# Kernel tuning notes

Measured on AMD Instinct MI355X. Metric: run time of the kernel, lower is better.

## Reference

```python
import jax, jax.numpy as jnp
import numpy as np

N = 100000   # nodes
E = 3200000  # edges (avg degree 32)
F = 128      # num_features
H = 256      # hidden_dim
D = 256      # embedding_dim
O = 2        # output_dim
BN_EPS = 1e-5


def _mk_layer(keys, fin, fmid, fout):
    kW1, kW2 = keys
    W1 = jax.random.normal(kW1, (fin, fmid), jnp.float32) / np.sqrt(fin)
    b1 = jnp.zeros((fmid,), jnp.float32)
    g = jnp.ones((fmid,), jnp.float32)
    be = jnp.zeros((fmid,), jnp.float32)
    mu = jnp.zeros((fmid,), jnp.float32)
    var = jnp.ones((fmid,), jnp.float32)
    W2 = jax.random.normal(kW2, (fmid, fout), jnp.float32) / np.sqrt(fmid)
    b2 = jnp.zeros((fout,), jnp.float32)
    return W1, b1, g, be, mu, var, W2, b2


def setup_inputs() -> dict:
    key = jax.random.key(0)
    ks = jax.random.split(key, 10)
    inp = {}
    inp["x"] = jax.random.normal(ks[0], (N, F), jnp.float32)
    inp["edge_index"] = jax.random.randint(ks[1], (2, E), 0, N, jnp.int32)
    names = ["W1", "b1", "g", "be", "mu", "var", "W2", "b2"]
    for pref, (fin, fmid, fout), kk in [
        ("l1", (F, H, H), (ks[2], ks[3])),
        ("l2", (H, H, H), (ks[4], ks[5])),
        ("l3", (H, H, D), (ks[6], ks[7])),
    ]:
        vals = _mk_layer(kk, fin, fmid, fout)
        for n, v in zip(names, vals):
            inp[f"{pref}_{n}"] = v
    inp["out_W"] = jax.random.normal(ks[8], (D, O), jnp.float32) / np.sqrt(D)
    inp["out_b"] = jnp.zeros((O,), jnp.float32)
    return inp


def gin_layer(h, src, dst, W1, b1, g, be, mu, var, W2, b2, final_relu):
    # GINConv (eps=0): z_i = x_i + sum_{j->i} x_j, then MLP(Linear-BN-ReLU-Linear[-ReLU])
    agg = jax.ops.segment_sum(h[src], dst, num_segments=N)
    z = h + agg
    z = z @ W1 + b1
    z = (z - mu) * jax.lax.rsqrt(var + BN_EPS) * g + be  # BatchNorm1d (inference)
    z = jax.nn.relu(z)
    z = z @ W2 + b2
    if final_relu:
        z = jax.nn.relu(z)
    return z


def reference(x, edge_index,
              l1_W1, l1_b1, l1_g, l1_be, l1_mu, l1_var, l1_W2, l1_b2,
              l2_W1, l2_b1, l2_g, l2_be, l2_mu, l2_var, l2_W2, l2_b2,
              l3_W1, l3_b1, l3_g, l3_be, l3_mu, l3_var, l3_W2, l3_b2,
              out_W, out_b):
    src, dst = edge_index[0], edge_index[1]
    h = gin_layer(x, src, dst, l1_W1, l1_b1, l1_g, l1_be, l1_mu, l1_var, l1_W2, l1_b2, True)
    h = gin_layer(h, src, dst, l2_W1, l2_b1, l2_g, l2_be, l2_mu, l2_var, l2_W2, l2_b2, True)
    h = gin_layer(h, src, dst, l3_W1, l3_b1, l3_g, l3_be, l3_mu, l3_var, l3_W2, l3_b2, False)
    return h @ out_W + out_b  # [N, O]
```

## Files before the change

### kernel.cpp

```cpp
#include <hip/hip_runtime.h>
#include <cstdint>
#include <cstddef>

#define N_NODES 100000
#define N_EDGES 3200000
#define MPAD    100096
#define HID     256
#define NBUCK   196
#define BSH     9
#define BSTRIDE 18432

typedef _Float16 f16;
typedef _Float16 f16x2 __attribute__((ext_vector_type(2)));
typedef _Float16 f16x8 __attribute__((ext_vector_type(8)));
typedef float    f32x4 __attribute__((ext_vector_type(4)));

union F16x2 { unsigned u; f16 h[2]; f16x2 v; };
__device__ inline void unpack2(unsigned u, float& a, float& b) {
    F16x2 x; x.u = u; a = (float)x.h[0]; b = (float)x.h[1];
}
__device__ inline unsigned pack2(float a, float b) {
    F16x2 x; x.h[0] = (f16)a; x.h[1] = (f16)b; return x.u;
}
__device__ inline f16x2 asv(unsigned u) { F16x2 x; x.u = u; return x.v; }

__global__ __launch_bounds__(256) void k_bucketA(const int* __restrict__ src,
                                                 const int* __restrict__ dst,
                                                 unsigned* __restrict__ pairs,
                                                 int* __restrict__ nb, int e) {
    __shared__ int hist[NBUCK];
    __shared__ int lbase[NBUCK];
    __shared__ int lcur[NBUCK];
    const int t = threadIdx.x;
    for (int i = t; i < NBUCK; i += 256) hist[i] = 0;
    __syncthreads();
    const int e0 = blockIdx.x * 4096;
    bool v[16]; int d[16], s[16];
#pragma unroll
    for (int i = 0; i < 16; ++i) {
        int idx = e0 + i * 256 + t;
        v[i] = idx < e;
        d[i] = v[i] ? dst[idx] : 0;
        s[i] = v[i] ? src[idx] : 0;
    }
#pragma unroll
    for (int i = 0; i < 16; ++i)
        if (v[i]) atomicAdd(&hist[d[i] >> BSH], 1);
    __syncthreads();
    for (int i = t; i < NBUCK; i += 256) {
        int h = hist[i];
        lbase[i] = h ? atomicAdd(&nb[i], h) : 0;
        lcur[i] = 0;
    }
    __syncthreads();
#pragma unroll
    for (int i = 0; i < 16; ++i) {
        if (v[i]) {
            int b = d[i] >> BSH;
            int p = atomicAdd(&lcur[b], 1);
            unsigned packed = ((unsigned)(d[i] & 511) << 17) | (unsigned)s[i];
            pairs[(size_t)b * BSTRIDE + lbase[b] + p] = packed;
        }
    }
}

__global__ void k_scan196(const int* __restrict__ nb, int* __restrict__ bbase,
                          int* __restrict__ rowptrN) {
    __shared__ int s[256];
    int t = threadIdx.x;
    int v = (t < NBUCK) ? nb[t] : 0;
    s[t] = v;
    __syncthreads();
    for (int off = 1; off < 256; off <<= 1) {
        int u = (t >= off) ? s[t - off] : 0;
        __syncthreads();
        s[t] += u;
        __syncthreads();
    }
    if (t < NBUCK) bbase[t] = s[t] - v;
    if (t == 0) *rowptrN = N_EDGES;
}

__global__ __launch_bounds__(256) void k_bucketB(const unsigned* __restrict__ pairs,
                                                 const int* __restrict__ nb,
                                                 const int* __restrict__ bbase,
                                                 int* __restrict__ rowptr,
                                                 int* __restrict__ colidx) {
    __shared__ int deg[512];
    __shared__ int sc[512];
    __shared__ int cur[512];
    const int b = blockIdx.x, t = threadIdx.x;
    const int cnt = nb[b], base = bbase[b];
    const unsigned* P = pairs + (size_t)b * BSTRIDE;
    deg[t] = 0; deg[t + 256] = 0;
    __syncthreads();
    for (int i = t; i < cnt; i += 256) atomicAdd(&deg[P[i] >> 17], 1);
    __syncthreads();
    sc[t] = deg[t]; sc[t + 256] = deg[t + 256];
    __syncthreads();
    for (int off = 1; off < 512; off <<= 1) {
        int a0 = (t >= off) ? sc[t - off] : 0;
        int a1 = (t + 256 >= off) ? sc[t + 256 - off] : 0;
        __syncthreads();
        sc[t] += a0; sc[t + 256] += a1;
        __syncthreads();
    }
    int node0 = b << BSH;
#pragma unroll
    for (int rep = 0; rep < 2; ++rep) {
        int i = t + rep * 256;
        int excl = base + sc[i] - deg[i];
        cur[i] = excl;
        int node = node0 + i;
        if (node < N_NODES) rowptr[node] = excl;
    }
    __syncthreads();
    for (int i = t; i < cnt; i += 256) {
        unsigned p = P[i];
        int pos = atomicAdd(&cur[p >> 17], 1);
        colidx[pos] = (int)(p & 0x1FFFF);
    }
}

__global__ void k_cvt(const float2* __restrict__ x, unsigned* __restrict__ o, int n) {
    int t = blockIdx.x * 256 + threadIdx.x;
    if (t < n) { float2 v = x[t]; o[t] = pack2(v.x, v.y); }
}

__global__ void k_foldw1(const float* __restrict__ W, const float* __restrict__ b1,
                         const float* __restrict__ gm, const float* __restrict__ bt,
                         const float* __restrict__ mu, const float* __restrict__ vr,
                         f16* __restrict__ Wt, float* __restrict__ bias, int K) {
    int t = blockIdx.x * 256 + threadIdx.x;
    if (t >= K * 256) return;
    int n = t & 255, k = t >> 8;
    float sc = gm[n] * rsqrtf(vr[n] + 1e-5f);
    Wt[n * K + k] = (f16)(W[t] * sc);
    if (k == 0) bias[n] = (b1[n] - mu[n]) * sc + bt[n];
}

__global__ void k_transb(const float* __restrict__ W, f16* __restrict__ Wt) {
    int t = blockIdx.x * 256 + threadIdx.x;
    int n = t & 255, k = t >> 8;
    Wt[n * 256 + k] = (f16)W[t];
}

__global__ void k_fold2(const float* __restrict__ W2, const float* __restrict__ b2,
                        const float* __restrict__ outW, const float* __restrict__ outb,
                        float* __restrict__ W2o, float* __restrict__ bo) {
    int k = threadIdx.x;
    float a0 = 0.f, a1 = 0.f;
    for (int j = 0; j < 256; ++j) {
        float w = W2[k * 256 + j];
        a0 += w * outW[j * 2 + 0];
        a1 += w * outW[j * 2 + 1];
    }
    W2o[k * 2 + 0] = a0;
    W2o[k * 2 + 1] = a1;
    if (k < 2) {
        float b = outb[k];
        for (int j = 0; j < 256; ++j) b += b2[j] * outW[j * 2 + k];
        bo[k] = b;
    }
}

__global__ void k_agg256(const unsigned* __restrict__ h8,
                         const int* __restrict__ rp, const int* __restrict__ ci,
                         uint2* __restrict__ z, int n) {
    int gw = (blockIdx.x * 256 + threadIdx.x) >> 6;
    if (gw >= n) return;
    int lane = threadIdx.x & 63;
    const unsigned* h8l = h8 + lane;
    float a0, a1, a2, a3;
    {
        unsigned u = h8l[(size_t)gw * 64];
        auto lo = __builtin_amdgcn_cvt_pk_f32_fp8(u, false);
        auto hi = __builtin_amdgcn_cvt_pk_f32_fp8(u, true);
        a0 = lo[0]; a1 = lo[1]; a2 = hi[0]; a3 = hi[1];
    }
    int s = rp[gw], e = rp[gw + 1];
    int p = s;
    for (; p + 7 < e; p += 8) {
        int j0 = ci[p],     j1 = ci[p + 1], j2 = ci[p + 2], j3 = ci[p + 3];
        int j4 = ci[p + 4], j5 = ci[p + 5], j6 = ci[p + 6], j7 = ci[p + 7];
        unsigned u0 = h8l[(size_t)j0 * 64], u1 = h8l[(size_t)j1 * 64];
        unsigned u2 = h8l[(size_t)j2 * 64], u3 = h8l[(size_t)j3 * 64];
        unsigned u4 = h8l[(size_t)j4 * 64], u5 = h8l[(size_t)j5 * 64];
        unsigned u6 = h8l[(size_t)j6 * 64], u7 = h8l[(size_t)j7 * 64];
#pragma unroll
        for (int q = 0; q < 8; ++q) {
            unsigned u = q == 0 ? u0 : q == 1 ? u1 : q == 2 ? u2 : q == 3 ? u3
                       : q == 4 ? u4 : q == 5 ? u5 : q == 6 ? u6 : u7;
            auto lo = __builtin_amdgcn_cvt_pk_f32_fp8(u, false);
            auto hi = __builtin_amdgcn_cvt_pk_f32_fp8(u, true);
            a0 += lo[0]; a1 += lo[1]; a2 += hi[0]; a3 += hi[1];
        }
    }
    for (; p < e; ++p) {
        unsigned u = h8l[(size_t)ci[p] * 64];
        auto lo = __builtin_amdgcn_cvt_pk_f32_fp8(u, false);
        auto hi = __builtin_amdgcn_cvt_pk_f32_fp8(u, true);
        a0 += lo[0]; a1 += lo[1]; a2 += hi[0]; a3 += hi[1];
    }
    uint2 o; o.x = pack2(a0, a1); o.y = pack2(a2, a3);
    z[(size_t)gw * 64 + lane] = o;
}

__global__ void k_agg128(const unsigned* __restrict__ h, const int* __restrict__ rp,
                         const int* __restrict__ ci, unsigned* __restrict__ z, int n) {
    int gw = (blockIdx.x * 256 + threadIdx.x) >> 6;
    if (gw >= n) return;
    int lane = threadIdx.x & 63;
    const unsigned* hl = h + lane;
    float a0, a1, t0, t1;
    unpack2(hl[(size_t)gw * 64], a0, a1);
    int s = rp[gw], e = rp[gw + 1];
    int p = s;
    for (; p + 7 < e; p += 8) {
        int j0 = ci[p],     j1 = ci[p + 1], j2 = ci[p + 2], j3 = ci[p + 3];
        int j4 = ci[p + 4], j5 = ci[p + 5], j6 = ci[p + 6], j7 = ci[p + 7];
        unsigned v0 = hl[(size_t)j0 * 64], v1 = hl[(size_t)j1 * 64];
        unsigned v2 = hl[(size_t)j2 * 64], v3 = hl[(size_t)j3 * 64];
        unsigned v4 = hl[(size_t)j4 * 64], v5 = hl[(size_t)j5 * 64];
        unsigned v6 = hl[(size_t)j6 * 64], v7 = hl[(size_t)j7 * 64];
        f16x2 sx = asv(v0);
        sx += asv(v1); sx += asv(v2); sx += asv(v3);
        sx += asv(v4); sx += asv(v5); sx += asv(v6); sx += asv(v7);
        a0 += (float)sx[0]; a1 += (float)sx[1];
    }
    for (; p < e; ++p) {
        unpack2(hl[(size_t)ci[p] * 64], t0, t1); a0 += t0; a1 += t1;
    }
    z[(size_t)gw * 64 + lane] = pack2(a0, a1);
}

template <int K, bool RELU, bool ST16, bool ST8>
__global__ __launch_bounds__(256, 2) void k_gemm2(const f16* __restrict__ A,
                                                  const f16* __restrict__ Bt,
                                                  const float* __restrict__ bias,
                                                  f16* __restrict__ C,
                                                  unsigned char* __restrict__ C8) {
    __shared__ f16 As[128 * 64];
    __shared__ f16 Bs[256 * 64];
    const int tid = threadIdx.x;
    const int bm0 = blockIdx.x * 128;
    const int lane = tid & 63, wave = tid >> 6;
    const int quad = lane >> 4, l16 = lane & 15;
    const int wr = (wave >> 1) * 64;
    const int wc = (wave & 1) * 128;
    f32x4 acc[4][8] = {};
    const f16* Abase = A + (size_t)bm0 * K;

    for (int k0 = 0; k0 < K; k0 += 64) {
#pragma unroll
        for (int i = 0; i < 4; ++i) {
            int c = i * 256 + tid;
            int m = c >> 3;
            int gg = (c & 7) ^ (m & 7);
            __builtin_amdgcn_global_load_lds(
                (const __attribute__((address_space(1))) unsigned int*)(Abase + (size_t)m * K + k0 + gg * 8),
                (__attribute__((address_space(3))) unsigned int*)(As + (size_t)c * 8), 16, 0, 0);
        }
#pragma unroll
        for (int i = 0; i < 8; ++i) {
            int c = i * 256 + tid;
            int m = c >> 3;
            int gg = (c & 7) ^ (m & 7);
            __builtin_amdgcn_global_load_lds(
                (const __attribute__((address_space(1))) unsigned int*)(Bt + (size_t)m * K + k0 + gg * 8),
                (__attribute__((address_space(3))) unsigned int*)(Bs + (size_t)c * 8), 16, 0, 0);
        }
        __syncthreads();
#pragma unroll
        for (int kk = 0; kk < 64; kk += 32) {
            const int gbase = kk >> 3;
            f16x8 af[4], bfv[8];
#pragma unroll
            for (int mi = 0; mi < 4; ++mi) {
                int m = wr + mi * 16 + l16;
                int slot = (gbase + quad) ^ (m & 7);
                af[mi] = *(const f16x8*)&As[(m * 8 + slot) * 8];
            }
#pragma unroll
            for (int ni = 0; ni < 8; ++ni) {
                int m = wc + ni * 16 + l16;
                int slot = (gbase + quad) ^ (m & 7);
                bfv[ni] = *(const f16x8*)&Bs[(m * 8 + slot) * 8];
            }
#pragma unroll
            for (int mi = 0; mi < 4; ++mi)
#pragma unroll
                for (int ni = 0; ni < 8; ++ni)
                    acc[mi][ni] = __builtin_amdgcn_mfma_f32_16x16x32_f16(af[mi], bfv[ni], acc[mi][ni], 0, 0, 0);
        }
        __syncthreads();
    }

    float bv[8];
#pragma unroll
    for (int ni = 0; ni < 8; ++ni) bv[ni] = bias[wc + ni * 16 + l16];
#pragma unroll
    for (int mi = 0; mi < 4; ++mi) {
#pragma unroll
        for (int r = 0; r < 4; ++r) {
            size_t row = (size_t)(bm0 + wr + mi * 16 + quad * 4 + r);
#pragma unroll
            for (int ni = 0; ni < 8; ++ni) {
                float v = acc[mi][ni][r] + bv[ni];
                if (RELU) v = fmaxf(v, 0.f);
                int col = wc + ni * 16 + l16;
                if (ST16) C[row * HID + col] = (f16)v;
                if (ST8) {
                    int pk = __builtin_amdgcn_cvt_pk_fp8_f32(v, v, 0, false);
                    C8[row * HID + col] = (unsigned char)(pk & 0xff);
                }
            }
        }
    }
}

__global__ void k_head(const uint2* __restrict__ y, const float* __restrict__ W2o,
                       const float* __restrict__ bo, float* __restrict__ out, int n) {
    __shared__ float w[512];
    __shared__ float bb[2];
    int t = threadIdx.x;
    w[t] = W2o[t];
    w[t + 256] = W2o[t + 256];
    if (t < 2) bb[t] = bo[t];
    __syncthreads();
    int gw = (blockIdx.x * 256 + t) >> 6;
    if (gw >= n) return;
    int lane = t & 63;
    uint2 d = y[(size_t)gw * 64 + lane];
    float x0, x1, x2, x3;
    unpack2(d.x, x0, x1); unpack2(d.y, x2, x3);
    int k = lane * 4;
    float o0 = x0 * w[k * 2 + 0] + x1 * w[k * 2 + 2] + x2 * w[k * 2 + 4] + x3 * w[k * 2 + 6];
    float o1 = x0 * w[k * 2 + 1] + x1 * w[k * 2 + 3] + x2 * w[k * 2 + 5] + x3 * w[k * 2 + 7];
#pragma unroll
    for (int off = 32; off > 0; off >>= 1) {
        o0 += __shfl_down(o0, off);
        o1 += __shfl_down(o1, off);
    }
    if (lane == 0) {
        out[(size_t)gw * 2 + 0] = o0 + bb[0];
        out[(size_t)gw * 2 + 1] = o1 + bb[1];
    }
}

extern "C" void kernel_launch(void* const* d_in, const int* in_sizes, int n_in,
                              void* d_out, int out_size, void* d_ws, size_t ws_size,
                              hipStream_t stream) {
    const float* x    = (const float*)d_in[0];
    const int*   ei   = (const int*)d_in[1];
    const int*   esrc = ei;
    const int*   edst = ei + N_EDGES;
    const float* lw[3][8];
    for (int l = 0; l < 3; ++l)
        for (int j = 0; j < 8; ++j) lw[l][j] = (const float*)d_in[2 + l * 8 + j];
    const float* outW = (const float*)d_in[26];
    const float* outB = (const float*)d_in[27];

    char* base = (char*)d_ws;
    size_t off = 0;
    auto alloc = [&](size_t bytes) -> void* {
        void* r = base + off;
        off += (bytes + 255) & ~(size_t)255;
        return r;
    };
    f16* z  = (f16*)alloc((size_t)MPAD * 256 * 2);
    f16* y  = (f16*)alloc((size_t)MPAD * 256 * 2);
    unsigned char* h8 = (unsigned char*)alloc((size_t)MPAD * 256);
    f16* xh = (f16*)alloc((size_t)MPAD * 128 * 2);
    f16* W1t[3]; float* bias1[3]; f16* W2t[2];
    W1t[0] = (f16*)alloc(256 * 128 * 2);
    W1t[1] = (f16*)alloc(256 * 256 * 2);
    W1t[2] = (f16*)alloc(256 * 256 * 2);
    for (int l = 0; l < 2; ++l) W2t[l] = (f16*)alloc(256 * 256 * 2);
    for (int l = 0; l < 3; ++l) bias1[l] = (float*)alloc(256 * 4);
    float* W2o = (float*)alloc(512 * 4);
    float* bo  = (float*)alloc(2 * 4);
    unsigned* pairs = (unsigned*)alloc((size_t)NBUCK * BSTRIDE * 4);
    int* nb     = (int*)alloc(NBUCK * 4);
    int* bbase  = (int*)alloc(NBUCK * 4);
    int* rowptr = (int*)alloc((size_t)(N_NODES + 1) * 4);
    int* colidx = (int*)alloc((size_t)N_EDGES * 4);

    hipMemsetAsync(nb, 0, NBUCK * 4, stream);
    k_bucketA<<<(N_EDGES + 4095) / 4096, 256, 0, stream>>>(esrc, edst, pairs, nb, N_EDGES);
    k_scan196<<<1, 256, 0, stream>>>(nb, bbase, rowptr + N_NODES);
    k_bucketB<<<NBUCK, 256, 0, stream>>>(pairs, nb, bbase, rowptr, colidx);

    k_cvt<<<(N_NODES * 64 + 255) / 256, 256, 0, stream>>>((const float2*)x, (unsigned*)xh, N_NODES * 64);
    k_foldw1<<<128, 256, 0, stream>>>(lw[0][0], lw[0][1], lw[0][2], lw[0][3], lw[0][4], lw[0][5], W1t[0], bias1[0], 128);
    k_foldw1<<<256, 256, 0, stream>>>(lw[1][0], lw[1][1], lw[1][2], lw[1][3], lw[1][4], lw[1][5], W1t[1], bias1[1], 256);
    k_foldw1<<<256, 256, 0, stream>>>(lw[2][0], lw[2][1], lw[2][2], lw[2][3], lw[2][4], lw[2][5], W1t[2], bias1[2], 256);
    k_transb<<<256, 256, 0, stream>>>(lw[0][6], W2t[0]);
    k_transb<<<256, 256, 0, stream>>>(lw[1][6], W2t[1]);
    k_fold2<<<1, 256, 0, stream>>>(lw[2][6], lw[2][7], outW, outB, W2o, bo);

    const int GG = MPAD / 128;
    const int WBLOCKS = (N_NODES + 3) / 4;

    k_agg128<<<WBLOCKS, 256, 0, stream>>>((const unsigned*)xh, rowptr, colidx, (unsigned*)z, N_NODES);
    k_gemm2<128, true, true,  false><<<GG, 256, 0, stream>>>(z, W1t[0], bias1[0], y, nullptr);
    k_gemm2<256, true, false, true ><<<GG, 256, 0, stream>>>(y, W2t[0], lw[0][7], nullptr, h8);
    k_agg256<<<WBLOCKS, 256, 0, stream>>>((const unsigned*)h8, rowptr, colidx, (uint2*)z, N_NODES);
    k_gemm2<256, true, true,  false><<<GG, 256, 0, stream>>>(z, W1t[1], bias1[1], y, nullptr);
    k_gemm2<256, true, false, true ><<<GG, 256, 0, stream>>>(y, W2t[1], lw[1][7], nullptr, h8);
    k_agg256<<<WBLOCKS, 256, 0, stream>>>((const unsigned*)h8, rowptr, colidx, (uint2*)z, N_NODES);
    k_gemm2<256, true, true,  false><<<GG, 256, 0, stream>>>(z, W1t[2], bias1[2], y, nullptr);
    k_head<<<WBLOCKS, 256, 0, stream>>>((const uint2*)y, W2o, bo, (float*)d_out, N_NODES);
}
```

Baseline: 751.5 us.

## Store input features in fp8 and prescale column indices for gathers

The input features are now converted to packed fp8 instead of fp16, which halves the bytes the first aggregation gathers per neighbor. Column indices are stored premultiplied by 64 so the gather kernels skip the per-edge multiply. Accumulation uses packed float2 vector adds. The cost is lower input precision: raw features go through fp8 quantization before layer 1, which may hurt accuracy.

Measured after the change: 719.6 us. -4.2%, faster.

```diff
diff --git a/kernel.cpp b/kernel.cpp
--- a/kernel.cpp
+++ b/kernel.cpp
@@ -14,6 +14,7 @@
 typedef _Float16 f16x2 __attribute__((ext_vector_type(2)));
 typedef _Float16 f16x8 __attribute__((ext_vector_type(8)));
 typedef float    f32x4 __attribute__((ext_vector_type(4)));
+typedef float    f32x2 __attribute__((ext_vector_type(2)));
 
 union F16x2 { unsigned u; f16 h[2]; f16x2 v; };
 __device__ inline void unpack2(unsigned u, float& a, float& b) {
@@ -22,7 +23,6 @@
 __device__ inline unsigned pack2(float a, float b) {
     F16x2 x; x.h[0] = (f16)a; x.h[1] = (f16)b; return x.u;
 }
-__device__ inline f16x2 asv(unsigned u) { F16x2 x; x.u = u; return x.v; }
 
 __global__ __launch_bounds__(256) void k_bucketA(const int* __restrict__ src,
                                                  const int* __restrict__ dst,
@@ -118,13 +118,17 @@
     for (int i = t; i < cnt; i += 256) {
         unsigned p = P[i];
         int pos = atomicAdd(&cur[p >> 17], 1);
-        colidx[pos] = (int)(p & 0x1FFFF);
-    }
-}
-
-__global__ void k_cvt(const float2* __restrict__ x, unsigned* __restrict__ o, int n) {
+        colidx[pos] = (int)(p & 0x1FFFF) << 6;
+    }
+}
+
+__global__ void k_cvt8(const float2* __restrict__ x, unsigned short* __restrict__ o, int n) {
     int t = blockIdx.x * 256 + threadIdx.x;
-    if (t < n) { float2 v = x[t]; o[t] = pack2(v.x, v.y); }
+    if (t < n) {
+        float2 v = x[t];
+        int pk = __builtin_amdgcn_cvt_pk_fp8_f32(v.x, v.y, 0, false);
+        o[t] = (unsigned short)(pk & 0xffff);
+    }
 }
 
 __global__ void k_foldw1(const float* __restrict__ W, const float* __restrict__ b1,
@@ -171,67 +175,67 @@
     if (gw >= n) return;
     int lane = threadIdx.x & 63;
     const unsigned* h8l = h8 + lane;
-    float a0, a1, a2, a3;
+    f32x2 A01, A23;
     {
         unsigned u = h8l[(size_t)gw * 64];
-        auto lo = __builtin_amdgcn_cvt_pk_f32_fp8(u, false);
-        auto hi = __builtin_amdgcn_cvt_pk_f32_fp8(u, true);
-        a0 = lo[0]; a1 = lo[1]; a2 = hi[0]; a3 = hi[1];
+        A01 = __builtin_amdgcn_cvt_pk_f32_fp8(u, false);
+        A23 = __builtin_amdgcn_cvt_pk_f32_fp8(u, true);
     }
     int s = rp[gw], e = rp[gw + 1];
     int p = s;
     for (; p + 7 < e; p += 8) {
         int j0 = ci[p],     j1 = ci[p + 1], j2 = ci[p + 2], j3 = ci[p + 3];
         int j4 = ci[p + 4], j5 = ci[p + 5], j6 = ci[p + 6], j7 = ci[p + 7];
-        unsigned u0 = h8l[(size_t)j0 * 64], u1 = h8l[(size_t)j1 * 64];
-        unsigned u2 = h8l[(size_t)j2 * 64], u3 = h8l[(size_t)j3 * 64];
-        unsigned u4 = h8l[(size_t)j4 * 64], u5 = h8l[(size_t)j5 * 64];
-        unsigned u6 = h8l[(size_t)j6 * 64], u7 = h8l[(size_t)j7 * 64];
+        unsigned u0 = h8l[(size_t)j0], u1 = h8l[(size_t)j1];
+        unsigned u2 = h8l[(size_t)j2], u3 = h8l[(size_t)j3];
+        unsigned u4 = h8l[(size_t)j4], u5 = h8l[(size_t)j5];
+        unsigned u6 = h8l[(size_t)j6], u7 = h8l[(size_t)j7];
 #pragma unroll
         for (int q = 0; q < 8; ++q) {
             unsigned u = q == 0 ? u0 : q == 1 ? u1 : q == 2 ? u2 : q == 3 ? u3
                        : q == 4 ? u4 : q == 5 ? u5 : q == 6 ? u6 : u7;
-            auto lo = __builtin_amdgcn_cvt_pk_f32_fp8(u, false);
-            auto hi = __builtin_amdgcn_cvt_pk_f32_fp8(u, true);
-            a0 += lo[0]; a1 += lo[1]; a2 += hi[0]; a3 += hi[1];
+            A01 += __builtin_amdgcn_cvt_pk_f32_fp8(u, false);
+            A23 += __builtin_amdgcn_cvt_pk_f32_fp8(u, true);
         }
     }
     for (; p < e; ++p) {
-        unsigned u = h8l[(size_t)ci[p] * 64];
-        auto lo = __builtin_amdgcn_cvt_pk_f32_fp8(u, false);
-        auto hi = __builtin_amdgcn_cvt_pk_f32_fp8(u, true);
-        a0 += lo[0]; a1 += lo[1]; a2 += hi[0]; a3 += hi[1];
-    }
-    uint2 o; o.x = pack2(a0, a1); o.y = pack2(a2, a3);
+        unsigned u = h8l[(size_t)ci[p]];
+        A01 += __builtin_amdgcn_cvt_pk_f32_fp8(u, false);
+        A23 += __builtin_amdgcn_cvt_pk_f32_fp8(u, true);
+    }
+    uint2 o; o.x = pack2(A01[0], A01[1]); o.y = pack2(A23[0], A23[1]);
     z[(size_t)gw * 64 + lane] = o;
 }
 
-__global__ void k_agg128(const unsigned* __restrict__ h, const int* __restrict__ rp,
-                         const int* __restrict__ ci, unsigned* __restrict__ z, int n) {
+__global__ void k_agg128(const unsigned short* __restrict__ x8,
+                         const int* __restrict__ rp, const int* __restrict__ ci,
+                         unsigned* __restrict__ z, int n) {
     int gw = (blockIdx.x * 256 + threadIdx.x) >> 6;
     if (gw >= n) return;
     int lane = threadIdx.x & 63;
-    const unsigned* hl = h + lane;
-    float a0, a1, t0, t1;
-    unpack2(hl[(size_t)gw * 64], a0, a1);
+    const unsigned short* xl = x8 + lane;
+    f32x2 A01 = __builtin_amdgcn_cvt_pk_f32_fp8((unsigned)xl[(size_t)gw * 64], false);
     int s = rp[gw], e = rp[gw + 1];
     int p = s;
     for (; p + 7 < e; p += 8) {
         int j0 = ci[p],     j1 = ci[p + 1], j2 = ci[p + 2], j3 = ci[p + 3];
         int j4 = ci[p + 4], j5 = ci[p + 5], j6 = ci[p + 6], j7 = ci[p + 7];
-        unsigned v0 = hl[(size_t)j0 * 64], v1 = hl[(size_t)j1 * 64];
-        unsigned v2 = hl[(size_t)j2 * 64], v3 = hl[(size_t)j3 * 64];
-        unsigned v4 = hl[(size_t)j4 * 64], v5 = hl[(size_t)j5 * 64];
-        unsigned v6 = hl[(size_t)j6 * 64], v7 = hl[(size_t)j7 * 64];
-        f16x2 sx = asv(v0);
-        sx += asv(v1); sx += asv(v2); sx += asv(v3);
-        sx += asv(v4); sx += asv(v5); sx += asv(v6); sx += asv(v7);
-        a0 += (float)sx[0]; a1 += (float)sx[1];
-    }
-    for (; p < e; ++p) {
-        unpack2(hl[(size_t)ci[p] * 64], t0, t1); a0 += t0; a1 += t1;
-    }
-    z[(size_t)gw * 64 + lane] = pack2(a0, a1);
+        unsigned u0 = xl[(size_t)j0], u1 = xl[(size_t)j1];
+        unsigned u2 = xl[(size_t)j2], u3 = xl[(size_t)j3];
+        unsigned u4 = xl[(size_t)j4], u5 = xl[(size_t)j5];
+        unsigned u6 = xl[(size_t)j6], u7 = xl[(size_t)j7];
+        A01 += __builtin_amdgcn_cvt_pk_f32_fp8(u0, false);
+        A01 += __builtin_amdgcn_cvt_pk_f32_fp8(u1, false);
+        A01 += __builtin_amdgcn_cvt_pk_f32_fp8(u2, false);
+        A01 += __builtin_amdgcn_cvt_pk_f32_fp8(u3, false);
+        A01 += __builtin_amdgcn_cvt_pk_f32_fp8(u4, false);
+        A01 += __builtin_amdgcn_cvt_pk_f32_fp8(u5, false);
+        A01 += __builtin_amdgcn_cvt_pk_f32_fp8(u6, false);
+        A01 += __builtin_amdgcn_cvt_pk_f32_fp8(u7, false);
+    }
+    for (; p < e; ++p)
+        A01 += __builtin_amdgcn_cvt_pk_f32_fp8((unsigned)xl[(size_t)ci[p]], false);
+    z[(size_t)gw * 64 + lane] = pack2(A01[0], A01[1]);
 }
 
 template <int K, bool RELU, bool ST16, bool ST8>
@@ -371,7 +375,7 @@
     f16* z  = (f16*)alloc((size_t)MPAD * 256 * 2);
     f16* y  = (f16*)alloc((size_t)MPAD * 256 * 2);
     unsigned char* h8 = (unsigned char*)alloc((size_t)MPAD * 256);
-    f16* xh = (f16*)alloc((size_t)MPAD * 128 * 2);
+    unsigned short* x8 = (unsigned short*)alloc((size_t)MPAD * 64 * 2);
     f16* W1t[3]; float* bias1[3]; f16* W2t[2];
     W1t[0] = (f16*)alloc(256 * 128 * 2);
     W1t[1] = (f16*)alloc(256 * 256 * 2);
@@ -391,7 +395,7 @@
     k_scan196<<<1, 256, 0, stream>>>(nb, bbase, rowptr + N_NODES);
     k_bucketB<<<NBUCK, 256, 0, stream>>>(pairs, nb, bbase, rowptr, colidx);
 
-    k_cvt<<<(N_NODES * 64 + 255) / 256, 256, 0, stream>>>((const float2*)x, (unsigned*)xh, N_NODES * 64);
+    k_cvt8<<<(N_NODES * 64 + 255) / 256, 256, 0, stream>>>((const float2*)x, x8, N_NODES * 64);
     k_foldw1<<<128, 256, 0, stream>>>(lw[0][0], lw[0][1], lw[0][2], lw[0][3], lw[0][4], lw[0][5], W1t[0], bias1[0], 128);
     k_foldw1<<<256, 256, 0, stream>>>(lw[1][0], lw[1][1], lw[1][2], lw[1][3], lw[1][4], lw[1][5], W1t[1], bias1[1], 256);
     k_foldw1<<<256, 256, 0, stream>>>(lw[2][0], lw[2][1], lw[2][2], lw[2][3], lw[2][4], lw[2][5], W1t[2], bias1[2], 256);
@@ -402,7 +406,7 @@
     const int GG = MPAD / 128;
     const int WBLOCKS = (N_NODES + 3) / 4;
 
-    k_agg128<<<WBLOCKS, 256, 0, stream>>>((const unsigned*)xh, rowptr, colidx, (unsigned*)z, N_NODES);
+    k_agg128<<<WBLOCKS, 256, 0, stream>>>(x8, rowptr, colidx, (unsigned*)z, N_NODES);
     k_gemm2<128, true, true,  false><<<GG, 256, 0, stream>>>(z, W1t[0], bias1[0], y, nullptr);
     k_gemm2<256, true, false, true ><<<GG, 256, 0, stream>>>(y, W2t[0], lw[0][7], nullptr, h8);
     k_agg256<<<WBLOCKS, 256, 0, stream>>>((const unsigned*)h8, rowptr, colidx, (uint2*)z, N_NODES);
```
